# Performance work log

Measured on AMD Instinct MI355X. Metric: run time of the kernel, lower is better.

Reference implementation:

```python
import jax
import jax.numpy as jnp
import numpy as np

# Periodic-boundary copy indices on the padded 18x18 lattice (dst <- src).
# None of the sources is an earlier destination, so one batched gather/scatter is faithful.
DST_R = np.array([1,1,2,3,4,4,6,7,8,10,11,12,14,14,15,16,17,17,16,15,14,14,12,10,8,6,4,4,3,2])
DST_C = np.array([3,5,7,9,10,11,13,13,14,15,15,16,15,16,15,14,13,11,9,7,6,5,3,2,1,0,0,1,1,2])
SRC_R = np.array([13,13,14,15,16,16,6,7,8,10,11,12,2,2,3,4,5,5,4,3,2,2,12,10,8,6,16,16,15,14])
SRC_C = np.array([15,5,7,9,10,11,1,1,2,3,3,4,3,4,3,2,1,11,9,7,6,5,15,14,13,12,12,13,13,14])

# 4x4 kernel sparsity masks (5 taps each)
_UP = np.zeros((4,4), np.float32);    _UP[[0,0,1,2,2],[0,1,1,1,2]] = 1
_LEFT = np.zeros((4,4), np.float32);  _LEFT[[1,2,2,2,3],[1,0,1,2,1]] = 1
_RIGHT = np.zeros((4,4), np.float32); _RIGHT[[1,2,2,2,3],[1,1,2,3,3]] = 1

def _out_mask():
    m = np.ones((16,16), np.float32)
    for i in range(9):
        m[i, 7+i:16] = 0
    for i in range(7):
        m[9+i, 0:i+1] = 0
    m[0,4:7]=0; m[1,6:8]=0; m[2,8]=0; m[3,9]=0
    m[6,12]=0; m[7,13]=0; m[8,14]=0; m[9,14]=0; m[10,14]=0; m[11,15]=0
    m[13:,14:]=0; m[15,13]=0; m[15,7:9]=0; m[13,5]=0; m[14,6]=0
    m[8,0]=0; m[9,1]=0; m[7,0]=0; m[3,0]=0; m[0:3,0:2]=0; m[0,2]=0
    return m
OUT_MASK = _out_mask()

def _conv(x, w, b):
    # kernel 4, stride 2, no padding: [B,C,18,18] -> [B,O,8,8]
    y = jax.lax.conv_general_dilated(x, w, window_strides=(2,2), padding='VALID',
                                     dimension_numbers=('NCHW','OIHW','NCHW'))
    return y + b[None, :, None, None]

def setup_inputs() -> dict:
    key = jax.random.key(0)
    ks = jax.random.split(key, 7)
    B, C, O = 2048, 64, 64
    x = jax.random.normal(ks[0], (B, C, 16, 16), dtype=jnp.float32)
    w_up = jax.random.normal(ks[1], (O, C, 4, 4), dtype=jnp.float32) * 0.05
    b_up = jax.random.normal(ks[2], (O,), dtype=jnp.float32) * 0.05
    w_left = jax.random.normal(ks[3], (O, C, 4, 4), dtype=jnp.float32) * 0.05
    b_left = jax.random.normal(ks[4], (O,), dtype=jnp.float32) * 0.05
    w_right = jax.random.normal(ks[5], (O, C, 4, 4), dtype=jnp.float32) * 0.05
    b_right = jax.random.normal(ks[6], (O,), dtype=jnp.float32) * 0.05
    return {"x": x, "w_up": w_up, "b_up": b_up, "w_left": w_left,
            "b_left": b_left, "w_right": w_right, "b_right": b_right}

def reference(x, w_up, b_up, w_left, b_left, w_right, b_right):
    # 1) zero-pad to 18x18 and apply periodic-boundary indexed copies
    xp = jnp.pad(x, ((0,0),(0,0),(1,1),(1,1)))
    xp = xp.at[:, :, DST_R, DST_C].set(xp[:, :, SRC_R, SRC_C])
    # 2) masked directional convs [B,O,8,8]
    up = _conv(xp, w_up * jnp.asarray(_UP), b_up)
    left = _conv(xp, w_left * jnp.asarray(_LEFT), b_left)
    right = _conv(xp, w_right * jnp.asarray(_RIGHT), b_right)
    # 3) interleave into 16x16: even rows = (up | 0) interleaved cols,
    #    odd rows = (left | right) interleaved cols
    B, O = up.shape[0], up.shape[1]
    out = jnp.zeros((B, O, 16, 16), x.dtype)
    out = out.at[:, :, 0::2, 0::2].set(up)
    out = out.at[:, :, 1::2, 0::2].set(left)
    out = out.at[:, :, 1::2, 1::2].set(right)
    # 4) static zero-out of non-lattice sites
    return out * jnp.asarray(OUT_MASK)
```

## Files before the change

### kernel.cpp

```cpp
#include <hip/hip_runtime.h>
#include <stdint.h>
#include <stddef.h>

typedef __attribute__((ext_vector_type(4))) float    f32x4;
typedef __attribute__((ext_vector_type(2))) float    f32x2;
typedef __attribute__((ext_vector_type(4))) uint32_t u32x4;
typedef __attribute__((ext_vector_type(8))) __bf16   bf16x8;

#define CGS   5200
#define NFRAG 15360

__device__ __constant__ uint8_t TAPR[15] = {0,0,1,2,2, 1,2,2,2,3, 1,2,2,2,3};
__device__ __constant__ uint8_t TAPC[15] = {0,1,1,1,2, 1,0,1,2,1, 1,1,2,3,3};

__device__ __constant__ uint8_t PDR[30] = {1,1,2,3,4,4,6,7,8,10,11,12,14,14,15,16,17,17,16,15,14,14,12,10,8,6,4,4,3,2};
__device__ __constant__ uint8_t PDC[30] = {3,5,7,9,10,11,13,13,14,15,15,16,15,16,15,14,13,11,9,7,6,5,3,2,1,0,0,1,1,2};
__device__ __constant__ uint8_t PSR[30] = {13,13,14,15,16,16,6,7,8,10,11,12,2,2,3,4,5,5,4,3,2,2,12,10,8,6,16,16,15,14};
__device__ __constant__ uint8_t PSC[30] = {15,5,7,9,10,11,1,1,2,3,3,4,3,4,3,2,1,11,9,7,6,5,15,14,13,12,12,13,13,14};

__global__ __launch_bounds__(256) void pack_w(const float* __restrict__ wu,
                                              const float* __restrict__ wl,
                                              const float* __restrict__ wr,
                                              uint16_t* __restrict__ pw) {
    int fid = blockIdx.x * 256 + threadIdx.x;
    if (fid >= NFRAG) return;
    int lane = fid & 63;
    int mt   = (fid >> 6) & 3;
    int kk   = (fid >> 8) & 1;
    int td   = fid >> 9;
    const float* w = (td < 5) ? wu : (td < 10) ? wl : wr;
    int o  = mt * 16 + (lane & 15);
    int cb = kk * 32 + (lane >> 4) * 8;
    int kr = TAPR[td], kc = TAPC[td];
    const float* src = w + ((size_t)o * 64 + cb) * 16 + kr * 4 + kc;
    uint32_t d[4];
#pragma unroll
    for (int p = 0; p < 4; ++p) {
        __bf16 h0 = (__bf16)src[(2 * p) * 16];
        __bf16 h1 = (__bf16)src[(2 * p + 1) * 16];
        d[p] = (uint32_t)__builtin_bit_cast(uint16_t, h0)
             | ((uint32_t)__builtin_bit_cast(uint16_t, h1) << 16);
    }
    u32x4 v = {d[0], d[1], d[2], d[3]};
    *(u32x4*)(pw + (size_t)fid * 8) = v;
}

__device__ __forceinline__ int slotof(int r, int c) { return (c & 1) * 162 + r * 9 + (c >> 1); }

__global__ __launch_bounds__(256, 2) void kagome_main(const float* __restrict__ x,
                                                      const uint16_t* __restrict__ pw,
                                                      const float* __restrict__ bu,
                                                      const float* __restrict__ bl,
                                                      const float* __restrict__ br,
                                                      float* __restrict__ out) {
    __shared__ __align__(16) uint8_t lds[8 * CGS];
    const int tid = threadIdx.x;
    const int b   = blockIdx.x;

    {
        const int px   = tid;
        const int prow = (px >> 4) + 1;
        const int pcol = (px & 15) + 1;
        const int slot = slotof(prow, pcol);
        const float* xb = x + (size_t)b * 16384 + px;
#pragma unroll
        for (int k = 0; k < 32; ++k) {
            float v0 = xb[(2 * k) * 256];
            float v1 = xb[(2 * k + 1) * 256];
            uint32_t u = (uint32_t)__builtin_bit_cast(uint16_t, (__bf16)v0)
                       | ((uint32_t)__builtin_bit_cast(uint16_t, (__bf16)v1) << 16);
            *(uint32_t*)(lds + (k >> 2) * CGS + slot * 16 + (k & 3) * 4) = u;
        }
        u32x4 z = {0, 0, 0, 0};
        for (int idx = tid; idx < 68 * 8; idx += 256) {
            int s = idx >> 3, cg = idx & 7;
            int r, c;
            if (s < 18)      { r = 0;  c = s; }
            else if (s < 36) { r = 17; c = s - 18; }
            else             { int k2 = s - 36; r = 1 + (k2 >> 1); c = (k2 & 1) * 17; }
            *(u32x4*)(lds + cg * CGS + slotof(r, c) * 16) = z;
        }
    }
    __syncthreads();
    if (tid < 240) {
        int pair = tid >> 3, cg = tid & 7;
        int sa = slotof(PSR[pair], PSC[pair]);
        int da = slotof(PDR[pair], PDC[pair]);
        u32x4 v = *(const u32x4*)(lds + cg * CGS + sa * 16);
        *(u32x4*)(lds + cg * CGS + da * 16) = v;
    }
    __syncthreads();

    const int l   = tid & 63;
    const int wid = tid >> 6;
    const int q   = l >> 4;
    const int io  = (l >> 3) & 1;
    const int j   = l & 7;

    f32x4 acc[3][4];
#pragma unroll
    for (int d2 = 0; d2 < 3; ++d2)
#pragma unroll
        for (int n2 = 0; n2 < 4; ++n2) acc[d2][n2] = (f32x4){0.f, 0.f, 0.f, 0.f};

    const int bbase = q * CGS + io * 288 + j * 16;
    const uint16_t* pwl = pw + (size_t)l * 8;

#pragma unroll
    for (int kk = 0; kk < 2; ++kk) {
        bf16x8 aw[15];
#pragma unroll
        for (int f2 = 0; f2 < 15; ++f2) {
            u32x4 t = *(const u32x4*)(pwl + (size_t)((f2 * 2 + kk) * 4 + wid) * 512);
            aw[f2] = __builtin_bit_cast(bf16x8, t);
        }
        const uint8_t* lb = lds + kk * (4 * CGS) + bbase;
#pragma unroll
        for (int nt = 0; nt < 4; ++nt) {
#define BRD(dr, dc) __builtin_bit_cast(bf16x8, *(const u32x4*)(lb + ((dc) & 1) * 2592 + (4 * nt + (dr)) * 144 + ((dc) >> 1) * 16))
            bf16x8 b00 = BRD(0, 0);
            acc[0][nt] = __builtin_amdgcn_mfma_f32_16x16x32_bf16(aw[0], b00, acc[0][nt], 0, 0, 0);
            bf16x8 b01 = BRD(0, 1);
            acc[0][nt] = __builtin_amdgcn_mfma_f32_16x16x32_bf16(aw[1], b01, acc[0][nt], 0, 0, 0);
            bf16x8 b11 = BRD(1, 1);
            acc[0][nt] = __builtin_amdgcn_mfma_f32_16x16x32_bf16(aw[2],  b11, acc[0][nt], 0, 0, 0);
            acc[1][nt] = __builtin_amdgcn_mfma_f32_16x16x32_bf16(aw[5],  b11, acc[1][nt], 0, 0, 0);
            acc[2][nt] = __builtin_amdgcn_mfma_f32_16x16x32_bf16(aw[10], b11, acc[2][nt], 0, 0, 0);
            bf16x8 b20 = BRD(2, 0);
            acc[1][nt] = __builtin_amdgcn_mfma_f32_16x16x32_bf16(aw[6],  b20, acc[1][nt], 0, 0, 0);
            bf16x8 b21 = BRD(2, 1);
            acc[0][nt] = __builtin_amdgcn_mfma_f32_16x16x32_bf16(aw[3],  b21, acc[0][nt], 0, 0, 0);
            acc[1][nt] = __builtin_amdgcn_mfma_f32_16x16x32_bf16(aw[7],  b21, acc[1][nt], 0, 0, 0);
            acc[2][nt] = __builtin_amdgcn_mfma_f32_16x16x32_bf16(aw[11], b21, acc[2][nt], 0, 0, 0);
            bf16x8 b22 = BRD(2, 2);
            acc[0][nt] = __builtin_amdgcn_mfma_f32_16x16x32_bf16(aw[4],  b22, acc[0][nt], 0, 0, 0);
            acc[1][nt] = __builtin_amdgcn_mfma_f32_16x16x32_bf16(aw[8],  b22, acc[1][nt], 0, 0, 0);
            acc[2][nt] = __builtin_amdgcn_mfma_f32_16x16x32_bf16(aw[12], b22, acc[2][nt], 0, 0, 0);
            bf16x8 b23 = BRD(2, 3);
            acc[2][nt] = __builtin_amdgcn_mfma_f32_16x16x32_bf16(aw[13], b23, acc[2][nt], 0, 0, 0);
            bf16x8 b31 = BRD(3, 1);
            acc[1][nt] = __builtin_amdgcn_mfma_f32_16x16x32_bf16(aw[9],  b31, acc[1][nt], 0, 0, 0);
            bf16x8 b33 = BRD(3, 3);
            acc[2][nt] = __builtin_amdgcn_mfma_f32_16x16x32_bf16(aw[14], b33, acc[2][nt], 0, 0, 0);
#undef BRD
        }
    }

    float bias0[4], bias1[4], bias2[4];
#pragma unroll
    for (int r = 0; r < 4; ++r) {
        int o = wid * 16 + q * 4 + r;
        bias0[r] = bu[o]; bias1[r] = bl[o]; bias2[r] = br[o];
    }

    constexpr uint32_t RM[16] = {0x0008, 0x003C, 0x00FC, 0x01FE, 0x07FF, 0x0FFF, 0x0FFF, 0x1FFE,
                                 0x3FFE, 0xBFFC, 0xBFFC, 0x7FF8, 0xFFF0, 0x3FC0, 0x3F80, 0x1E00};
#pragma unroll
    for (int nt = 0; nt < 4; ++nt) {
        const int row_e = 4 * nt + 2 * io;
        const uint32_t me = io ? RM[4 * nt + 2] : RM[4 * nt + 0];
        const uint32_t mo = io ? RM[4 * nt + 3] : RM[4 * nt + 1];
        const uint32_t be  = (me >> (2 * j)) & 1u;
        const uint32_t bo0 = (mo >> (2 * j)) & 1u;
        const uint32_t bo1 = (mo >> (2 * j + 1)) & 1u;
#pragma unroll
        for (int r = 0; r < 4; ++r) {
            int o = wid * 16 + q * 4 + r;
            float up = acc[0][nt][r] + bias0[r];
            float lf = acc[1][nt][r] + bias1[r];
            float rt = acc[2][nt][r] + bias2[r];
            up = be  ? up : 0.f;
            lf = bo0 ? lf : 0.f;
            rt = bo1 ? rt : 0.f;
            float* po = out + (((size_t)b * 64 + o) * 256 + row_e * 16 + 2 * j);
            *(f32x2*)po        = (f32x2){up, 0.f};
            *(f32x2*)(po + 16) = (f32x2){lf, rt};
        }
    }
}

extern "C" void kernel_launch(void* const* d_in, const int* in_sizes, int n_in,
                              void* d_out, int out_size, void* d_ws, size_t ws_size,
                              hipStream_t stream) {
    const float* x  = (const float*)d_in[0];
    const float* wu = (const float*)d_in[1];
    const float* bu = (const float*)d_in[2];
    const float* wl = (const float*)d_in[3];
    const float* bl = (const float*)d_in[4];
    const float* wr = (const float*)d_in[5];
    const float* br = (const float*)d_in[6];
    float* out   = (float*)d_out;
    uint16_t* pw = (uint16_t*)d_ws;

    int B = in_sizes[0] / 16384;
    pack_w<<<(NFRAG + 255) / 256, 256, 0, stream>>>(wu, wl, wr, pw);
    kagome_main<<<B, 256, 0, stream>>>(x, pw, bu, bl, br, out);
}
```

Measured before the change: 62.31 us.

## Vectorize input staging with float4 loads and 16-byte LDS stores; raise occupancy

The input staging loop now has each thread load float4 quads from 8 channels and write packed 16-byte LDS entries, replacing 64 scalar global loads and 32 scalar 4-byte LDS stores per thread. The intent is to cut global load instruction count and LDS store traffic in the prologue. Launch bounds also change from 2 to 3 blocks per SIMD-pair, which raises occupancy but may force register spills given the 8-register-wide vector buffers.

```diff
diff --git a/kernel.cpp b/kernel.cpp
--- a/kernel.cpp
+++ b/kernel.cpp
@@ -17,6 +17,11 @@
 __device__ __constant__ uint8_t PDC[30] = {3,5,7,9,10,11,13,13,14,15,15,16,15,16,15,14,13,11,9,7,6,5,3,2,1,0,0,1,1,2};
 __device__ __constant__ uint8_t PSR[30] = {13,13,14,15,16,16,6,7,8,10,11,12,2,2,3,4,5,5,4,3,2,2,12,10,8,6,16,16,15,14};
 __device__ __constant__ uint8_t PSC[30] = {15,5,7,9,10,11,1,1,2,3,3,4,3,4,3,2,1,11,9,7,6,5,15,14,13,12,12,13,13,14};
+
+__device__ __forceinline__ uint32_t pk2(float a, float b) {
+    return (uint32_t)__builtin_bit_cast(uint16_t, (__bf16)a)
+         | ((uint32_t)__builtin_bit_cast(uint16_t, (__bf16)b) << 16);
+}
 
 __global__ __launch_bounds__(256) void pack_w(const float* __restrict__ wu,
                                               const float* __restrict__ wl,
@@ -35,19 +40,15 @@
     const float* src = w + ((size_t)o * 64 + cb) * 16 + kr * 4 + kc;
     uint32_t d[4];
 #pragma unroll
-    for (int p = 0; p < 4; ++p) {
-        __bf16 h0 = (__bf16)src[(2 * p) * 16];
-        __bf16 h1 = (__bf16)src[(2 * p + 1) * 16];
-        d[p] = (uint32_t)__builtin_bit_cast(uint16_t, h0)
-             | ((uint32_t)__builtin_bit_cast(uint16_t, h1) << 16);
-    }
+    for (int p = 0; p < 4; ++p)
+        d[p] = pk2(src[(2 * p) * 16], src[(2 * p + 1) * 16]);
     u32x4 v = {d[0], d[1], d[2], d[3]};
     *(u32x4*)(pw + (size_t)fid * 8) = v;
 }
 
 __device__ __forceinline__ int slotof(int r, int c) { return (c & 1) * 162 + r * 9 + (c >> 1); }
 
-__global__ __launch_bounds__(256, 2) void kagome_main(const float* __restrict__ x,
+__global__ __launch_bounds__(256, 3) void kagome_main(const float* __restrict__ x,
                                                       const uint16_t* __restrict__ pw,
                                                       const float* __restrict__ bu,
                                                       const float* __restrict__ bl,
@@ -58,18 +59,27 @@
     const int b   = blockIdx.x;
 
     {
-        const int px   = tid;
-        const int prow = (px >> 4) + 1;
-        const int pcol = (px & 15) + 1;
-        const int slot = slotof(prow, pcol);
-        const float* xb = x + (size_t)b * 16384 + px;
-#pragma unroll
-        for (int k = 0; k < 32; ++k) {
-            float v0 = xb[(2 * k) * 256];
-            float v1 = xb[(2 * k + 1) * 256];
-            uint32_t u = (uint32_t)__builtin_bit_cast(uint16_t, (__bf16)v0)
-                       | ((uint32_t)__builtin_bit_cast(uint16_t, (__bf16)v1) << 16);
-            *(uint32_t*)(lds + (k >> 2) * CGS + slot * 16 + (k & 3) * 4) = u;
+        const float* xb = x + (size_t)b * 16384;
+#pragma unroll
+        for (int i = 0; i < 2; ++i) {
+            const int t    = i * 256 + tid;
+            const int cg   = t >> 6;
+            const int quad = t & 63;
+            const int r0   = quad >> 2;
+            const int qc   = quad & 3;
+            f32x4 v[8];
+#pragma unroll
+            for (int ch = 0; ch < 8; ++ch)
+                v[ch] = *(const f32x4*)(xb + (cg * 8 + ch) * 256 + quad * 4);
+            uint8_t* base = lds + cg * CGS;
+#pragma unroll
+            for (int e = 0; e < 4; ++e) {
+                const int pc   = 4 * qc + e + 1;
+                const int slot = slotof(r0 + 1, pc);
+                u32x4 w = {pk2(v[0][e], v[1][e]), pk2(v[2][e], v[3][e]),
+                           pk2(v[4][e], v[5][e]), pk2(v[6][e], v[7][e])};
+                *(u32x4*)(base + slot * 16) = w;
+            }
         }
         u32x4 z = {0, 0, 0, 0};
         for (int idx = tid; idx < 68 * 8; idx += 256) {
```

Measured after the change: 62.44 us. No clear change (+0.2%).
